# Performance work log

Measured on AMD Instinct MI355X. Metric: run time of the kernel, lower is better.

## Reference

```python
import jax, jax.numpy as jnp
import numpy as np

R = 2          # total_rel
N = 6144       # total_ent / num nodes
H1 = 256       # layer 1 out
H2 = 256       # layer 2 out


def setup_inputs() -> dict:
    key = jax.random.key(0)
    k_adj, k_w1, k_c1, k_w2, k_c2 = jax.random.split(key, 5)
    adj = jax.random.uniform(k_adj, (R, N, N), dtype=jnp.float32)
    bw1 = jax.random.normal(k_w1, (R, N, H1), dtype=jnp.float32) * (1.0 / np.sqrt(N))
    bc1 = jax.random.normal(k_c1, (R, R), dtype=jnp.float32)
    bw2 = jax.random.normal(k_w2, (R, H1, H2), dtype=jnp.float32) * (1.0 / np.sqrt(H1))
    bc2 = jax.random.normal(k_c2, (R, R), dtype=jnp.float32)
    return {"adj": adj, "bw1": bw1, "bc1": bc1, "bw2": bw2, "bc2": bc2}


def _layer_weights(coeff, basis):
    # (R, n_basis) x (n_basis, in, out) -> (R*in, out)
    w = jnp.einsum('ij,jmn->imn', coeff, basis)
    return w.reshape(w.shape[0] * w.shape[1], w.shape[2])


def reference(adj, bw1, bc1, bw2, bc2):
    # --- layer 1: node_init is None -> features are dense adjacencies ---
    w1 = _layer_weights(bc1, bw1)                        # (R*N, H1)
    # cat([adj[0], adj[1]], axis=1) == transpose+reshape  (N, R*N)
    tmp1 = adj.transpose(1, 0, 2).reshape(N, R * N)
    out1 = tmp1 @ w1                                     # (N, H1)

    # --- layer 2: relu then per-relation spmm + basis matmul ---
    x = jax.nn.relu(out1)
    w2 = _layer_weights(bc2, bw2)                        # (R*H1, H2)
    # cat([adj[r] @ x for r], axis=1) as one einsum       (N, R*H1)
    tmp2 = jnp.einsum('rij,jd->ird', adj, x).reshape(N, R * H1)
    out2 = tmp2 @ w2                                     # (N, H2)

    final_rep = jnp.concatenate([out1, out2], axis=1)    # (N, H1+H2)
    final_rep = jnp.sum(final_rep, axis=0).reshape(-1, H1 + H2)  # (1, H1+H2)
    return (out2, final_rep)
```

## Files before the change

kernel.cpp:

```cpp
#include <hip/hip_runtime.h>


#define NN 6144
#define HH 256
#define SPLIT 8
#define KCHUNK 1536
#define KSTEPS 24

typedef __attribute__((ext_vector_type(4))) float f32x4;
typedef __attribute__((ext_vector_type(8))) unsigned short u16x8;
typedef __attribute__((ext_vector_type(4))) unsigned short u16x4;

__device__ __forceinline__ unsigned short f2bf(float f) {
  unsigned int u = __float_as_uint(f);
  u += 0x7FFFu + ((u >> 16) & 1u);
  return (unsigned short)(u >> 16);
}
__device__ __forceinline__ float bf2f(unsigned short h) {
  return __uint_as_float(((unsigned int)h) << 16);
}

__device__ __forceinline__ void mfma_bf16(f32x4& d, u16x8 a, u16x8 b) {
  asm("v_mfma_f32_16x16x32_bf16 %0, %1, %2, %0" : "+v"(d) : "v"(a), "v"(b));
}

#define BAR_PRE_STAGE()   asm volatile("s_barrier" ::: "memory")
#define BAR_PRE_COMPUTE() asm volatile("s_waitcnt lgkmcnt(0)\n\ts_barrier" ::: "memory")

__global__ void prep_kernel(const float* __restrict__ bw1, const float* __restrict__ bc1,
                            const float* __restrict__ bw2, const float* __restrict__ bc2,
                            unsigned short* __restrict__ B1ws, unsigned short* __restrict__ w2ws,
                            float* __restrict__ fin)
{
  const int b   = blockIdx.x;
  const int tid = threadIdx.x;
  if (b >= 200) { fin[(b - 200) * 256 + tid] = 0.f; return; }

  const float* basis; const float* bc; unsigned short* outw;
  int tilesPerR, jdim, t;
  if (b < 192) { basis = bw1; bc = bc1; outw = B1ws; tilesPerR = 96; jdim = NN; t = b; }
  else         { basis = bw2; bc = bc2; outw = w2ws; tilesPerR = 4;  jdim = HH; t = b - 192; }

  __shared__ unsigned short wt[64][265];
  const int r  = t / tilesPerR;
  const int jt = t % tilesPerR;
  const float c0 = bc[r * 2 + 0];
  const float c1 = bc[r * 2 + 1];
  const float* b0 = basis + (size_t)jt * 64 * HH;
  const float* b1 = basis + (size_t)jdim * HH + (size_t)jt * 64 * HH;
#pragma unroll
  for (int k = 0; k < 16; ++k) {
    int idx = tid + k * 256;
    int row = idx >> 6;
    int c4  = (idx & 63) * 4;
    f32x4 v0 = *(const f32x4*)(b0 + (size_t)row * HH + c4);
    f32x4 v1 = *(const f32x4*)(b1 + (size_t)row * HH + c4);
    wt[row][c4 + 0] = f2bf(c0 * v0.x + c1 * v1.x);
    wt[row][c4 + 1] = f2bf(c0 * v0.y + c1 * v1.y);
    wt[row][c4 + 2] = f2bf(c0 * v0.z + c1 * v1.z);
    wt[row][c4 + 3] = f2bf(c0 * v0.w + c1 * v1.w);
  }
  __syncthreads();
#pragma unroll
  for (int k = 0; k < 8; ++k) {
    int chunk = tid + k * 256;
    int h  = chunk >> 3;
    int sp = chunk & 7;
    int j0 = (sp ^ (h & 7)) * 8;
    u16x8 v;
#pragma unroll
    for (int e = 0; e < 8; ++e) v[e] = wt[j0 + e][h];
    *(u16x8*)(outw + ((size_t)t * 2048 + chunk) * 8) = v;
  }
}

__global__ __launch_bounds__(256, 3) void gemm_adj_kernel(
    const float* __restrict__ adj, const unsigned short* __restrict__ Bws,
    unsigned short* __restrict__ Pp)
{
  __shared__ __align__(16) unsigned short Alds[64 * 64];
  __shared__ __align__(16) unsigned short Blds[256 * 64];
  const int tid  = threadIdx.x;
  const int lane = tid & 63;
  const int wave = tid >> 6;
  const int bid  = blockIdx.x;
  const int s    = bid & 7;
  const int mb   = bid >> 3;
  const int i0 = mb * 64;
  const int kbase = s * KCHUNK;
  const int rrel  = kbase / NN;
  const int jb    = kbase % NN;
  const int tBase = kbase / 64;

  const float* aRow = adj + (size_t)rrel * NN * NN
                      + (size_t)(i0 + (tid >> 4)) * NN + jb + (tid & 15) * 4;
  const unsigned short* bBase = Bws + (size_t)tBase * 2048 * 8 + (size_t)tid * 8;

  f32x4 acc[4][4];
#pragma unroll
  for (int m = 0; m < 4; ++m)
#pragma unroll
    for (int n = 0; n < 4; ++n) acc[m][n] = (f32x4){0.f, 0.f, 0.f, 0.f};

  f32x4 av0[4], av1[4];
  u16x8 bv[8];

#define ISSUE_A(SET, KK) do {                                                  \
    _Pragma("unroll")                                                          \
    for (int it = 0; it < 4; ++it)                                             \
      SET[it] = *(const f32x4*)(aRow + (size_t)it * 16 * NN + (KK) * 64);      \
  } while (0)

#define ISSUE_B(KK) do {                                                       \
    _Pragma("unroll")                                                          \
    for (int c = 0; c < 8; ++c)                                                \
      bv[c] = *(const u16x8*)(bBase + (size_t)(KK) * 2048 * 8 + c * 256 * 8);  \
  } while (0)

#define STAGE_A(SET) do {                                                      \
    _Pragma("unroll")                                                          \
    for (int it = 0; it < 4; ++it) {                                           \
      int row = (tid >> 4) + it * 16;                                          \
      int off = ((tid & 15) * 8) ^ ((row & 7) << 4);                           \
      u16x4 w;                                                                 \
      w[0] = f2bf(SET[it].x); w[1] = f2bf(SET[it].y);                          \
      w[2] = f2bf(SET[it].z); w[3] = f2bf(SET[it].w);                          \
      *(u16x4*)((char*)Alds + row * 128 + off) = w;                            \
    } } while (0)

#define STAGE_B() do {                                                         \
    _Pragma("unroll")                                                          \
    for (int c = 0; c < 8; ++c)                                                \
      *(u16x8*)(Blds + ((size_t)c * 256 + tid) * 8) = bv[c];                   \
  } while (0)

#define COMPUTE() do {                                                         \
    _Pragma("unroll")                                                          \
    for (int ks = 0; ks < 2; ++ks) {                                           \
      u16x8 af[4], bfr[4];                                                     \
      _Pragma("unroll")                                                        \
      for (int m = 0; m < 4; ++m) {                                            \
        int row = m * 16 + (lane & 15);                                        \
        int off = (ks * 64 + ((lane >> 4) << 4)) ^ ((row & 7) << 4);           \
        af[m] = *(const u16x8*)((const char*)Alds + row * 128 + off);          \
      }                                                                        \
      _Pragma("unroll")                                                        \
      for (int n = 0; n < 4; ++n) {                                            \
        int row = wave * 64 + n * 16 + (lane & 15);                            \
        int off = (ks * 64 + ((lane >> 4) << 4)) ^ ((row & 7) << 4);           \
        bfr[n] = *(const u16x8*)((const char*)Blds + row * 128 + off);         \
      }                                                                        \
      _Pragma("unroll")                                                        \
      for (int m = 0; m < 4; ++m)                                              \
        _Pragma("unroll")                                                      \
        for (int n = 0; n < 4; ++n)                                            \
          mfma_bf16(acc[m][n], af[m], bfr[n]);                                 \
    } } while (0)

  ISSUE_A(av0, 0);
  ISSUE_A(av1, 1);
  ISSUE_B(0);

  for (int kk = 0; kk < KSTEPS; kk += 2) {
    BAR_PRE_STAGE();
    STAGE_A(av0);
    STAGE_B();
    BAR_PRE_COMPUTE();
    ISSUE_B(kk + 1);
    COMPUTE();
    BAR_PRE_STAGE();
    STAGE_A(av1);
    STAGE_B();
    BAR_PRE_COMPUTE();
    if (kk + 2 < KSTEPS) {
      ISSUE_A(av0, kk + 2);
      ISSUE_A(av1, kk + 3);
      ISSUE_B(kk + 2);
    }
    COMPUTE();
  }
#undef ISSUE_A
#undef ISSUE_B
#undef STAGE_A
#undef STAGE_B
#undef COMPUTE

  unsigned short* P = Pp + ((size_t)s * NN + i0) * HH;
#pragma unroll
  for (int m = 0; m < 4; ++m)
#pragma unroll
    for (int n = 0; n < 4; ++n) {
      int col = wave * 64 + n * 16 + (lane & 15);
#pragma unroll
      for (int q = 0; q < 4; ++q) {
        int row = m * 16 + ((lane >> 4) << 2) + q;
        P[(size_t)row * HH + col] = f2bf(acc[m][n][q]);
      }
    }
}

__global__ __launch_bounds__(256, 2) void gemm_y_kernel(
    const unsigned short* __restrict__ xws, const unsigned short* __restrict__ w2ws,
    unsigned short* __restrict__ B2ws)
{
  __shared__ __align__(16) unsigned short Alds[64 * 64];
  __shared__ __align__(16) unsigned short Blds[256 * 64];
  const int tid  = threadIdx.x;
  const int lane = tid & 63;
  const int wave = tid >> 6;
  const int mb = blockIdx.x;
  const int r  = blockIdx.y;

  f32x4 acc[4][4];
#pragma unroll
  for (int m = 0; m < 4; ++m)
#pragma unroll
    for (int n = 0; n < 4; ++n) acc[m][n] = (f32x4){0.f, 0.f, 0.f, 0.f};

  for (int dt = 0; dt < 4; ++dt) {
    u16x8 avv[2];
    avv[0] = *(const u16x8*)(xws + (((size_t)(mb * 4 + dt)) * 512 + tid) * 8);
    avv[1] = *(const u16x8*)(xws + (((size_t)(mb * 4 + dt)) * 512 + 256 + tid) * 8);
    u16x8 bv[8];
#pragma unroll
    for (int c = 0; c < 8; ++c)
      bv[c] = *(const u16x8*)(w2ws + (((size_t)(r * 4 + dt)) * 2048 + c * 256 + tid) * 8);
    __syncthreads();
    *(u16x8*)(Alds + (size_t)tid * 8) = avv[0];
    *(u16x8*)(Alds + ((size_t)256 + tid) * 8) = avv[1];
#pragma unroll
    for (int c = 0; c < 8; ++c)
      *(u16x8*)(Blds + ((size_t)c * 256 + tid) * 8) = bv[c];
    __syncthreads();
#pragma unroll
    for (int ks = 0; ks < 2; ++ks) {
      u16x8 af[4], bfr[4];
#pragma unroll
      for (int m = 0; m < 4; ++m) {
        int row = m * 16 + (lane & 15);
        int off = (ks * 64 + ((lane >> 4) << 4)) ^ ((row & 7) << 4);
        af[m] = *(const u16x8*)((const char*)Alds + row * 128 + off);
      }
#pragma unroll
      for (int n = 0; n < 4; ++n) {
        int row = wave * 64 + n * 16 + (lane & 15);
        int off = (ks * 64 + ((lane >> 4) << 4)) ^ ((row & 7) << 4);
        bfr[n] = *(const u16x8*)((const char*)Blds + row * 128 + off);
      }
#pragma unroll
      for (int m = 0; m < 4; ++m)
#pragma unroll
        for (int n = 0; n < 4; ++n)
          mfma_bf16(acc[m][n], af[m], bfr[n]);
    }
  }
  const int tg = r * 96 + mb;
#pragma unroll
  for (int m = 0; m < 4; ++m) {
    int scont = m * 2 + ((lane >> 4) >> 1);
    int e0    = ((lane >> 4) & 1) * 4;
#pragma unroll
    for (int n = 0; n < 4; ++n) {
      int h   = wave * 64 + n * 16 + (lane & 15);
      int pos = scont ^ (h & 7);
      u16x4 v;
      v[0] = f2bf(acc[m][n][0]); v[1] = f2bf(acc[m][n][1]);
      v[2] = f2bf(acc[m][n][2]); v[3] = f2bf(acc[m][n][3]);
      *(u16x4*)(B2ws + (((size_t)tg * 2048 + h * 8 + pos) * 8 + e0)) = v;
    }
  }
}

__global__ void reduce1_kernel(const unsigned short* __restrict__ Pp,
                               unsigned short* __restrict__ xws,
                               float* __restrict__ fin)
{
  __shared__ float csm[8][256];
  const int tid = threadIdx.x;
  const int b   = blockIdx.x;
  const int hc  = tid & 31;
  const int rg  = tid >> 5;
  const int dt    = hc >> 3;
  const int scont = hc & 7;
  float cs[8] = {0.f, 0.f, 0.f, 0.f, 0.f, 0.f, 0.f, 0.f};
  for (int k = 0; k < 8; ++k) {
    int i = b * 64 + rg + k * 8;
    float sv[8] = {0.f, 0.f, 0.f, 0.f, 0.f, 0.f, 0.f, 0.f};
#pragma unroll
    for (int s = 0; s < SPLIT; ++s) {
      u16x8 v = *(const u16x8*)(Pp + ((size_t)s * NN + i) * HH + hc * 8);
#pragma unroll
      for (int e = 0; e < 8; ++e) sv[e] += bf2f(v[e]);
    }
    u16x8 xv;
#pragma unroll
    for (int e = 0; e < 8; ++e) {
      cs[e] += sv[e];
      xv[e] = f2bf(fmaxf(sv[e], 0.f));
    }
    int pos = scont ^ (i & 7);
    *(u16x8*)(xws + (((size_t)(b * 4 + dt)) * 512 + (i & 63) * 8 + pos) * 8) = xv;
  }
#pragma unroll
  for (int e = 0; e < 8; ++e) csm[rg][hc * 8 + e] = cs[e];
  __syncthreads();
  float v = 0.f;
#pragma unroll
  for (int r8 = 0; r8 < 8; ++r8) v += csm[r8][tid];
  atomicAdd(&fin[tid], v);
}

__global__ void reduce2_kernel(const unsigned short* __restrict__ Pp,
                               float* __restrict__ outp,
                               float* __restrict__ fin)
{
  __shared__ float csm[8][256];
  const int tid = threadIdx.x;
  const int b   = blockIdx.x;
  const int hc  = tid & 31;
  const int rg  = tid >> 5;
  float cs[8] = {0.f, 0.f, 0.f, 0.f, 0.f, 0.f, 0.f, 0.f};
  for (int k = 0; k < 8; ++k) {
    int i = b * 64 + rg + k * 8;
    float sv[8] = {0.f, 0.f, 0.f, 0.f, 0.f, 0.f, 0.f, 0.f};
#pragma unroll
    for (int s = 0; s < SPLIT; ++s) {
      u16x8 v = *(const u16x8*)(Pp + ((size_t)s * NN + i) * HH + hc * 8);
#pragma unroll
      for (int e = 0; e < 8; ++e) sv[e] += bf2f(v[e]);
    }
    float* o = outp + (size_t)i * HH + hc * 8;
    *(f32x4*)o = (f32x4){sv[0], sv[1], sv[2], sv[3]};
    *(f32x4*)(o + 4) = (f32x4){sv[4], sv[5], sv[6], sv[7]};
#pragma unroll
    for (int e = 0; e < 8; ++e) cs[e] += sv[e];
  }
#pragma unroll
  for (int e = 0; e < 8; ++e) csm[rg][hc * 8 + e] = cs[e];
  __syncthreads();
  float v = 0.f;
#pragma unroll
  for (int r8 = 0; r8 < 8; ++r8) v += csm[r8][tid];
  atomicAdd(&fin[256 + tid], v);
}

extern "C" void kernel_launch(void* const* d_in, const int* in_sizes, int n_in,
                              void* d_out, int out_size, void* d_ws, size_t ws_size,
                              hipStream_t stream)
{
  const float* adj = (const float*)d_in[0];
  const float* bw1 = (const float*)d_in[1];
  const float* bc1 = (const float*)d_in[2];
  const float* bw2 = (const float*)d_in[3];
  const float* bc2 = (const float*)d_in[4];
  float* out2 = (float*)d_out;
  float* fin  = (float*)d_out + (size_t)NN * HH;

  char* ws = (char*)d_ws;
  unsigned short* Pp   = (unsigned short*)(ws + 0);
  unsigned short* B1ws = (unsigned short*)(ws + 25165824);
  unsigned short* B2ws = (unsigned short*)(ws + 31457280);
  unsigned short* xws  = (unsigned short*)(ws + 37748736);
  unsigned short* w2ws = (unsigned short*)(ws + 40894464);

  prep_kernel<<<202, 256, 0, stream>>>(bw1, bc1, bw2, bc2, B1ws, w2ws, fin);
  gemm_adj_kernel<<<768, 256, 0, stream>>>(adj, B1ws, Pp);
  reduce1_kernel<<<96, 256, 0, stream>>>(Pp, xws, fin);
  gemm_y_kernel<<<dim3(96, 2), 256, 0, stream>>>(xws, w2ws, B2ws);
  gemm_adj_kernel<<<768, 256, 0, stream>>>(adj, B2ws, Pp);
  reduce2_kernel<<<96, 256, 0, stream>>>(Pp, out2, fin);
}
```

Measured before the change: 194.5 us.

## Cache bf16 adjacency tiles in workspace for reuse in second GEMM pass

The first adjacency GEMM now also writes its bf16-converted, swizzled A tiles to a workspace buffer. The second GEMM reads these tiles instead of the fp32 adjacency, halving its A-side read traffic and skipping the conversion. The cost is an extra 150 MB of writes in the first pass. The new path is used only when the workspace is large enough, otherwise the original kernels run.

Result: faster. 189.8 us (-2.4%).

```diff
diff --git a/kernel.cpp b/kernel.cpp
--- a/kernel.cpp
+++ b/kernel.cpp
@@ -74,59 +74,30 @@
   }
 }
 
-__global__ __launch_bounds__(256, 3) void gemm_adj_kernel(
-    const float* __restrict__ adj, const unsigned short* __restrict__ Bws,
-    unsigned short* __restrict__ Pp)
-{
-  __shared__ __align__(16) unsigned short Alds[64 * 64];
-  __shared__ __align__(16) unsigned short Blds[256 * 64];
-  const int tid  = threadIdx.x;
-  const int lane = tid & 63;
-  const int wave = tid >> 6;
-  const int bid  = blockIdx.x;
-  const int s    = bid & 7;
-  const int mb   = bid >> 3;
-  const int i0 = mb * 64;
-  const int kbase = s * KCHUNK;
-  const int rrel  = kbase / NN;
-  const int jb    = kbase % NN;
-  const int tBase = kbase / 64;
-
-  const float* aRow = adj + (size_t)rrel * NN * NN
-                      + (size_t)(i0 + (tid >> 4)) * NN + jb + (tid & 15) * 4;
+#define GEMM_PROLOGUE_COMMON()                                                 \
+  const int tid  = threadIdx.x;                                                \
+  const int lane = tid & 63;                                                   \
+  const int wave = tid >> 6;                                                   \
+  const int bid  = blockIdx.x;                                                 \
+  const int s    = bid & 7;                    \
+  const int mb   = bid >> 3;                                                   \
+  const int i0 = mb * 64;                                                      \
+  const int kbase = s * KCHUNK;                                                \
+  const int tBase = kbase / 64;                                                \
   const unsigned short* bBase = Bws + (size_t)tBase * 2048 * 8 + (size_t)tid * 8;
 
-  f32x4 acc[4][4];
-#pragma unroll
-  for (int m = 0; m < 4; ++m)
-#pragma unroll
+#define DECL_ACC()                                                             \
+  f32x4 acc[4][4];                                                             \
+  _Pragma("unroll")                                                            \
+  for (int m = 0; m < 4; ++m)                                                  \
+    _Pragma("unroll")                                                          \
     for (int n = 0; n < 4; ++n) acc[m][n] = (f32x4){0.f, 0.f, 0.f, 0.f};
-
-  f32x4 av0[4], av1[4];
-  u16x8 bv[8];
-
-#define ISSUE_A(SET, KK) do {                                                  \
-    _Pragma("unroll")                                                          \
-    for (int it = 0; it < 4; ++it)                                             \
-      SET[it] = *(const f32x4*)(aRow + (size_t)it * 16 * NN + (KK) * 64);      \
-  } while (0)
 
 #define ISSUE_B(KK) do {                                                       \
     _Pragma("unroll")                                                          \
     for (int c = 0; c < 8; ++c)                                                \
       bv[c] = *(const u16x8*)(bBase + (size_t)(KK) * 2048 * 8 + c * 256 * 8);  \
   } while (0)
-
-#define STAGE_A(SET) do {                                                      \
-    _Pragma("unroll")                                                          \
-    for (int it = 0; it < 4; ++it) {                                           \
-      int row = (tid >> 4) + it * 16;                                          \
-      int off = ((tid & 15) * 8) ^ ((row & 7) << 4);                           \
-      u16x4 w;                                                                 \
-      w[0] = f2bf(SET[it].x); w[1] = f2bf(SET[it].y);                          \
-      w[2] = f2bf(SET[it].z); w[3] = f2bf(SET[it].w);                          \
-      *(u16x4*)((char*)Alds + row * 128 + off) = w;                            \
-    } } while (0)
 
 #define STAGE_B() do {                                                         \
     _Pragma("unroll")                                                          \
@@ -157,19 +128,69 @@
           mfma_bf16(acc[m][n], af[m], bfr[n]);                                 \
     } } while (0)
 
+#define WRITE_P() do {                                                         \
+    unsigned short* P = Pp + ((size_t)s * NN + i0) * HH;                       \
+    _Pragma("unroll")                                                          \
+    for (int m = 0; m < 4; ++m)                                                \
+      _Pragma("unroll")                                                        \
+      for (int n = 0; n < 4; ++n) {                                            \
+        int col = wave * 64 + n * 16 + (lane & 15);                            \
+        _Pragma("unroll")                                                      \
+        for (int q = 0; q < 4; ++q) {                                          \
+          int row = m * 16 + ((lane >> 4) << 2) + q;                           \
+          P[(size_t)row * HH + col] = f2bf(acc[m][n][q]);                      \
+        }                                                                      \
+      } } while (0)
+
+#define ISSUE_A(SET, KK) do {                                                  \
+    _Pragma("unroll")                                                          \
+    for (int it = 0; it < 4; ++it)                                             \
+      SET[it] = *(const f32x4*)(aRow + (size_t)it * 16 * NN + (KK) * 64);      \
+  } while (0)
+
+__global__ __launch_bounds__(256, 3) void gemm_adj_store_kernel(
+    const float* __restrict__ adj, const unsigned short* __restrict__ Bws,
+    unsigned short* __restrict__ Pp, unsigned short* __restrict__ Aws)
+{
+  __shared__ __align__(16) unsigned short Alds[64 * 64];
+  __shared__ __align__(16) unsigned short Blds[256 * 64];
+  GEMM_PROLOGUE_COMMON();
+  const int rrel = kbase / NN;
+  const int jb   = kbase % NN;
+  const float* aRow = adj + (size_t)rrel * NN * NN
+                      + (size_t)(i0 + (tid >> 4)) * NN + jb + (tid & 15) * 4;
+  char* aTile0 = (char*)Aws + ((size_t)(s * 96 + mb) * 24) * 8192;
+
+  DECL_ACC();
+  f32x4 av0[4], av1[4];
+  u16x8 bv[8];
+
+#define STAGE_A_ST(SET, KK) do {                                               \
+    char* at = aTile0 + (size_t)(KK) * 8192;                                   \
+    _Pragma("unroll")                                                          \
+    for (int it = 0; it < 4; ++it) {                                           \
+      int row = (tid >> 4) + it * 16;                                          \
+      int off = ((tid & 15) * 8) ^ ((row & 7) << 4);                           \
+      u16x4 w;                                                                 \
+      w[0] = f2bf(SET[it].x); w[1] = f2bf(SET[it].y);                          \
+      w[2] = f2bf(SET[it].z); w[3] = f2bf(SET[it].w);                          \
+      *(u16x4*)((char*)Alds + row * 128 + off) = w;                            \
+      *(u16x4*)(at + row * 128 + off) = w;                                     \
+    } } while (0)
+
   ISSUE_A(av0, 0);
   ISSUE_A(av1, 1);
   ISSUE_B(0);
 
   for (int kk = 0; kk < KSTEPS; kk += 2) {
     BAR_PRE_STAGE();
-    STAGE_A(av0);
+    STAGE_A_ST(av0, kk);
     STAGE_B();
     BAR_PRE_COMPUTE();
     ISSUE_B(kk + 1);
     COMPUTE();
     BAR_PRE_STAGE();
-    STAGE_A(av1);
+    STAGE_A_ST(av1, kk + 1);
     STAGE_B();
     BAR_PRE_COMPUTE();
     if (kk + 2 < KSTEPS) {
@@ -179,24 +200,112 @@
     }
     COMPUTE();
   }
-#undef ISSUE_A
-#undef ISSUE_B
+#undef STAGE_A_ST
+  WRITE_P();
+}
+
+__global__ __launch_bounds__(256, 3) void gemm_adj_bf_kernel(
+    const unsigned short* __restrict__ Aws, const unsigned short* __restrict__ Bws,
+    unsigned short* __restrict__ Pp)
+{
+  __shared__ __align__(16) unsigned short Alds[64 * 64];
+  __shared__ __align__(16) unsigned short Blds[256 * 64];
+  GEMM_PROLOGUE_COMMON();
+  const char* aTile0 = (const char*)Aws + ((size_t)(s * 96 + mb) * 24) * 8192;
+
+  DECL_ACC();
+  u16x8 av0[2], av1[2];
+  u16x8 bv[8];
+
+#define ISSUE_A2(SET, KK) do {                                                 \
+    const char* at = aTile0 + (size_t)(KK) * 8192 + (size_t)tid * 32;          \
+    SET[0] = *(const u16x8*)(at);                                              \
+    SET[1] = *(const u16x8*)(at + 16);                                         \
+  } while (0)
+
+#define STAGE_A2(SET) do {                                                     \
+    *(u16x8*)((char*)Alds + (size_t)tid * 32) = SET[0];                        \
+    *(u16x8*)((char*)Alds + (size_t)tid * 32 + 16) = SET[1];                   \
+  } while (0)
+
+  ISSUE_A2(av0, 0);
+  ISSUE_A2(av1, 1);
+  ISSUE_B(0);
+
+  for (int kk = 0; kk < KSTEPS; kk += 2) {
+    BAR_PRE_STAGE();
+    STAGE_A2(av0);
+    STAGE_B();
+    BAR_PRE_COMPUTE();
+    ISSUE_B(kk + 1);
+    COMPUTE();
+    BAR_PRE_STAGE();
+    STAGE_A2(av1);
+    STAGE_B();
+    BAR_PRE_COMPUTE();
+    if (kk + 2 < KSTEPS) {
+      ISSUE_A2(av0, kk + 2);
+      ISSUE_A2(av1, kk + 3);
+      ISSUE_B(kk + 2);
+    }
+    COMPUTE();
+  }
+#undef ISSUE_A2
+#undef STAGE_A2
+  WRITE_P();
+}
+
+__global__ __launch_bounds__(256, 3) void gemm_adj_kernel(
+    const float* __restrict__ adj, const unsigned short* __restrict__ Bws,
+    unsigned short* __restrict__ Pp)
+{
+  __shared__ __align__(16) unsigned short Alds[64 * 64];
+  __shared__ __align__(16) unsigned short Blds[256 * 64];
+  GEMM_PROLOGUE_COMMON();
+  const int rrel = kbase / NN;
+  const int jb   = kbase % NN;
+  const float* aRow = adj + (size_t)rrel * NN * NN
+                      + (size_t)(i0 + (tid >> 4)) * NN + jb + (tid & 15) * 4;
+
+  DECL_ACC();
+  f32x4 av0[4], av1[4];
+  u16x8 bv[8];
+
+#define STAGE_A(SET) do {                                                      \
+    _Pragma("unroll")                                                          \
+    for (int it = 0; it < 4; ++it) {                                           \
+      int row = (tid >> 4) + it * 16;                                          \
+      int off = ((tid & 15) * 8) ^ ((row & 7) << 4);                           \
+      u16x4 w;                                                                 \
+      w[0] = f2bf(SET[it].x); w[1] = f2bf(SET[it].y);                          \
+      w[2] = f2bf(SET[it].z); w[3] = f2bf(SET[it].w);                          \
+      *(u16x4*)((char*)Alds + row * 128 + off) = w;                            \
+    } } while (0)
+
+  ISSUE_A(av0, 0);
+  ISSUE_A(av1, 1);
+  ISSUE_B(0);
+
+  for (int kk = 0; kk < KSTEPS; kk += 2) {
+    BAR_PRE_STAGE();
+    STAGE_A(av0);
+    STAGE_B();
+    BAR_PRE_COMPUTE();
+    ISSUE_B(kk + 1);
+    COMPUTE();
+    BAR_PRE_STAGE();
+    STAGE_A(av1);
+    STAGE_B();
+    BAR_PRE_COMPUTE();
+    if (kk + 2 < KSTEPS) {
+      ISSUE_A(av0, kk + 2);
+      ISSUE_A(av1, kk + 3);
+      ISSUE_B(kk + 2);
+    }
+    COMPUTE();
+  }
 #undef STAGE_A
-#undef STAGE_B
-#undef COMPUTE
-
-  unsigned short* P = Pp + ((size_t)s * NN + i0) * HH;
-#pragma unroll
-  for (int m = 0; m < 4; ++m)
-#pragma unroll
-    for (int n = 0; n < 4; ++n) {
-      int col = wave * 64 + n * 16 + (lane & 15);
-#pragma unroll
-      for (int q = 0; q < 4; ++q) {
-        int row = m * 16 + ((lane >> 4) << 2) + q;
-        P[(size_t)row * HH + col] = f2bf(acc[m][n][q]);
-      }
-    }
+  WRITE_P();
 }
 
 __global__ __launch_bounds__(256, 2) void gemm_y_kernel(
@@ -362,11 +471,19 @@
   unsigned short* B2ws = (unsigned short*)(ws + 31457280);
   unsigned short* xws  = (unsigned short*)(ws + 37748736);
   unsigned short* w2ws = (unsigned short*)(ws + 40894464);
+  unsigned short* Aws  = (unsigned short*)(ws + 41943040);
+  const bool handoff = (ws_size >= (size_t)192937984);
 
   prep_kernel<<<202, 256, 0, stream>>>(bw1, bc1, bw2, bc2, B1ws, w2ws, fin);
-  gemm_adj_kernel<<<768, 256, 0, stream>>>(adj, B1ws, Pp);
+  if (handoff)
+    gemm_adj_store_kernel<<<768, 256, 0, stream>>>(adj, B1ws, Pp, Aws);
+  else
+    gemm_adj_kernel<<<768, 256, 0, stream>>>(adj, B1ws, Pp);
   reduce1_kernel<<<96, 256, 0, stream>>>(Pp, xws, fin);
   gemm_y_kernel<<<dim3(96, 2), 256, 0, stream>>>(xws, w2ws, B2ws);
-  gemm_adj_kernel<<<768, 256, 0, stream>>>(adj, B2ws, Pp);
+  if (handoff)
+    gemm_adj_bf_kernel<<<768, 256, 0, stream>>>(Aws, B2ws, Pp);
+  else
+    gemm_adj_kernel<<<768, 256, 0, stream>>>(adj, B2ws, Pp);
   reduce2_kernel<<<96, 256, 0, stream>>>(Pp, out2, fin);
 }
```
